# Optimization experiments

Measured on AMD Instinct MI355X. Metric: run time of the kernel, lower is better.

## Reference

```python
import jax, jax.numpy as jnp
import numpy as np


def setup_inputs() -> dict:
    key = jax.random.key(0)
    kq, kk, kv = jax.random.split(key, 3)
    B, S, H, D = 2, 2048, 32, 128
    q = jax.random.normal(kq, (B, S, H, D), dtype=jnp.float32)
    k = jax.random.normal(kk, (B, S, H, D), dtype=jnp.float32)
    v = jax.random.normal(kv, (B, S, H, D), dtype=jnp.float32)
    return {"q": q, "k": k, "v": v}


def _causal_attention(q, k, v):
    # q,k,v: [B, S, H, D] (flash-attn layout). Zigzag ring attention computes
    # exactly standard causal attention; zigzag only balances work across ranks.
    B, S, H, D = q.shape
    scale = 1.0 / jnp.sqrt(jnp.asarray(D, q.dtype))
    scores = jnp.einsum('bqhd,bkhd->bhqk', q, k) * scale  # [B,H,S,S]
    causal = jnp.tril(jnp.ones((S, S), dtype=bool))
    scores = jnp.where(causal, scores, jnp.finfo(scores.dtype).min)
    probs = jax.nn.softmax(scores, axis=-1)
    return jnp.einsum('bhqk,bkhd->bqhd', probs, v)  # [B,S,H,D]


def reference(q, k, v):
    out = _causal_attention(q, k, v)
    return jnp.sum(out)
```

## Files before the change

kernel.cpp:

```cpp
#include <hip/hip_runtime.h>
#include <hip/hip_bf16.h>
#include <stdint.h>

#define B_ 2
#define S_ 2048
#define H_ 32
#define D_ 128
#define R_ (B_*H_*S_)
#define PG 2048
#define CPB 40

typedef __bf16 bf16x8 __attribute__((ext_vector_type(8)));
typedef float  f32x16 __attribute__((ext_vector_type(16)));

#if __has_builtin(__builtin_amdgcn_exp2f)
#define EXP2F(x) __builtin_amdgcn_exp2f(x)
#else
#define EXP2F(x) exp2f(x)
#endif

#define AS1 __attribute__((address_space(1)))
#define AS3 __attribute__((address_space(3)))

__device__ __forceinline__ unsigned short f2bf(float f) {
  unsigned u = __float_as_uint(f);
  u += 0x7FFFu + ((u >> 16) & 1u);
  return (unsigned short)(u >> 16);
}

__global__ __launch_bounds__(256) void prep(
    const float* __restrict__ qf, const float* __restrict__ kf,
    const float* __restrict__ v,
    unsigned short* __restrict__ qc, unsigned short* __restrict__ kc,
    float* __restrict__ vsum, float* __restrict__ nd, float* __restrict__ out0) {
  const int bid = blockIdx.x;
  const int t = threadIdx.x;
  if (bid == 0 && t == 0) out0[0] = 0.f;
  const float sc = 0.0883883476483184f * 1.4426950408889634f;

  #pragma unroll
  for (int g = 0; g < 4; ++g) {
    const size_t i = (size_t)g * (PG * 256) + (size_t)bid * 256 + t;
    const float4 a = *reinterpret_cast<const float4*>(qf + i * 8);
    const float4 b = *reinterpret_cast<const float4*>(qf + i * 8 + 4);
    union { unsigned short u[8]; uint4 v4; } o;
    o.u[0] = f2bf(a.x * sc); o.u[1] = f2bf(a.y * sc);
    o.u[2] = f2bf(a.z * sc); o.u[3] = f2bf(a.w * sc);
    o.u[4] = f2bf(b.x * sc); o.u[5] = f2bf(b.y * sc);
    o.u[6] = f2bf(b.z * sc); o.u[7] = f2bf(b.w * sc);
    *reinterpret_cast<uint4*>(qc + i * 8) = o.v4;
  }
  #pragma unroll
  for (int g = 0; g < 4; ++g) {
    const size_t i = (size_t)g * (PG * 256) + (size_t)bid * 256 + t;
    const float4 a = *reinterpret_cast<const float4*>(kf + i * 8);
    const float4 b = *reinterpret_cast<const float4*>(kf + i * 8 + 4);
    union { unsigned short u[8]; uint4 v4; } o;
    o.u[0] = f2bf(a.x); o.u[1] = f2bf(a.y);
    o.u[2] = f2bf(a.z); o.u[3] = f2bf(a.w);
    o.u[4] = f2bf(b.x); o.u[5] = f2bf(b.y);
    o.u[6] = f2bf(b.z); o.u[7] = f2bf(b.w);
    *reinterpret_cast<uint4*>(kc + i * 8) = o.v4;
  }

  #pragma unroll
  for (int g = 0; g < (B_ * S_) / PG; ++g) {
    const int u = bid + g * PG;
    const int b = u / S_, s = u % S_;
    const int h = t >> 3, i = t & 7;
    const float* p = v + (((size_t)b * S_ + s) * H_ + h) * D_ + i * 16;
    const float4 a0 = *reinterpret_cast<const float4*>(p + 0);
    const float4 a1 = *reinterpret_cast<const float4*>(p + 4);
    const float4 a2 = *reinterpret_cast<const float4*>(p + 8);
    const float4 a3 = *reinterpret_cast<const float4*>(p + 12);
    float sum = (a0.x+a0.y+a0.z+a0.w) + (a1.x+a1.y+a1.z+a1.w)
              + (a2.x+a2.y+a2.z+a2.w) + (a3.x+a3.y+a3.z+a3.w);
    sum += __shfl_xor(sum, 1);
    sum += __shfl_xor(sum, 2);
    sum += __shfl_xor(sum, 4);
    if (i == 0) vsum[((size_t)b * H_ + h) * S_ + s] = sum;
  }

  if (bid < 256) {
    float4* p = reinterpret_cast<float4*>(nd);
    p[(size_t)bid * 256 + t] = float4{0.f, 0.f, 0.f, 0.f};
  }
}

__global__ __launch_bounds__(256, 4) void attn_sum(
    const unsigned short* __restrict__ qc, const unsigned short* __restrict__ kc,
    const float* __restrict__ vsum, float* __restrict__ numb,
    float* __restrict__ denb) {
  __shared__ uint4 kbuf[4][512];
  __shared__ float vsbuf[4][64];

  const int id = blockIdx.x;
  const int y  = id >> 3;
  const int bh = (id & 7) + 8 * (y / CPB);
  const int c  = y % CPB;

  int qt, h, nch;
  if (c < 4)       { qt = c;                 h = 0;            nch = 1; }
  else if (c < 12) { qt = 4 + ((c - 4) >> 1);  h = (c - 4) & 1;  nch = 2; }
  else if (c < 24) { qt = 8 + (c - 12) / 3;    h = (c - 12) % 3; nch = 3; }
  else             { qt = 12 + ((c - 24) >> 2); h = (c - 24) & 3; nch = 4; }
  const int nkt  = 2 * qt + 2;
  const int bas_ = nkt / nch, rem = nkt % nch;
  const int kt0  = h * bas_ + (h < rem ? h : rem);
  const int kt1  = kt0 + bas_ + (h < rem ? 1 : 0);
  const int st0  = 2 * kt0, st1 = 2 * kt1;

  const int t  = threadIdx.x;
  const int w  = t >> 6;
  const int l  = t & 63;
  const int ln = l & 31, l5 = l >> 5;

  const int b0 = bh >> 5, h0 = bh & 31;
  const int qrow0 = qt * 128 + w * 32;
  const unsigned short* kc0 = kc + ((size_t)b0 * S_ * H_ + h0) * D_;
  const float* vsrc0 = vsum + (size_t)bh * S_;

  bf16x8 qfrag[8];
  {
    const unsigned short* qp =
        qc + (((size_t)b0 * S_ + qrow0 + ln) * H_ + h0) * D_ + l5 * 8;
    #pragma unroll
    for (int kb8 = 0; kb8 < 8; ++kb8)
      qfrag[kb8] = *reinterpret_cast<const bf16x8*>(qp + kb8 * 16);
  }

  auto stage = [&](int st, int slot) {
    #pragma unroll
    for (int j = 0; j < 2; ++j) {
      const int idx = (w * 2 + j) * 64 + l;
      const int r   = idx >> 4;
      const int p   = idx & 15;
      const int cc  = p ^ (r & 15);
      const unsigned short* src = kc0 + (size_t)(st * 32 + r) * (H_ * D_) + cc * 8;
      __builtin_amdgcn_global_load_lds(
          (const AS1 void*)src, (AS3 void*)(&kbuf[slot][idx & ~63]), 16, 0, 0);
    }
    __builtin_amdgcn_global_load_lds(
        (const AS1 void*)(vsrc0 + st * 32 + l), (AS3 void*)(&vsbuf[slot][0]), 4, 0, 0);
  };

  float num[16], den[16];
  #pragma unroll
  for (int r = 0; r < 16; ++r) { num[r] = 0.f; den[r] = 0.f; }

  stage(st0, st0 & 3);
  stage(st0 + 1, (st0 + 1) & 3);

  const int xr = ln & 15;
  for (int st = st0; st < st1; ++st) {
    if (st + 1 < st1) asm volatile("s_waitcnt vmcnt(3)" ::: "memory");
    else              asm volatile("s_waitcnt vmcnt(0)" ::: "memory");
    __builtin_amdgcn_s_barrier();
    if (st + 2 < st1) stage(st + 2, (st + 2) & 3);

    const int kbase = st * 32;
    if (kbase <= qrow0 + 31) {
      const int slot = st & 3;
      const uint4* rowb = &kbuf[slot][ln * 16];
      f32x16 sacc = {0.f,0.f,0.f,0.f,0.f,0.f,0.f,0.f,
                     0.f,0.f,0.f,0.f,0.f,0.f,0.f,0.f};
      __builtin_amdgcn_s_setprio(1);
      #pragma unroll
      for (int kb8 = 0; kb8 < 8; ++kb8) {
        const bf16x8 bf = *reinterpret_cast<const bf16x8*>(&rowb[(kb8 * 2 + l5) ^ xr]);
        sacc = __builtin_amdgcn_mfma_f32_32x32x16_bf16(qfrag[kb8], bf, sacc, 0, 0, 0);
      }
      __builtin_amdgcn_s_setprio(0);
      const float vsv = vsbuf[slot][ln];
      if (kbase + 31 <= qrow0) {
        #pragma unroll
        for (int r = 0; r < 16; ++r) {
          const float e = EXP2F(sacc[r]);
          den[r] += e;
          num[r] = fmaf(e, vsv, num[r]);
        }
      } else {
        const int kgc = kbase + ln;
        #pragma unroll
        for (int r = 0; r < 16; ++r) {
          const int qgr = qrow0 + (r & 3) + 8 * (r >> 2) + 4 * l5;
          const float e = (kgc <= qgr) ? EXP2F(sacc[r]) : 0.f;
          den[r] += e;
          num[r] = fmaf(e, vsv, num[r]);
        }
      }
    }
  }

  #pragma unroll
  for (int m = 1; m < 32; m <<= 1) {
    #pragma unroll
    for (int r = 0; r < 16; ++r) {
      num[r] += __shfl_xor(num[r], m);
      den[r] += __shfl_xor(den[r], m);
    }
  }
  if (ln == 0) {
    float* nrow = numb + (size_t)bh * S_;
    float* drow = denb + (size_t)bh * S_;
    #pragma unroll
    for (int r = 0; r < 16; ++r) {
      const int qgr = qrow0 + (r & 3) + 8 * (r >> 2) + 4 * l5;
      atomicAdd(&nrow[qgr], num[r]);
      atomicAdd(&drow[qgr], den[r]);
    }
  }
}

__global__ __launch_bounds__(256) void finalize(
    const float* __restrict__ numb, const float* __restrict__ denb,
    float* __restrict__ out) {
  const int i = blockIdx.x * 256 + threadIdx.x;
  float c = numb[i] / denb[i];
  #pragma unroll
  for (int m = 1; m < 64; m <<= 1) c += __shfl_xor(c, m);
  __shared__ float ps[4];
  if ((threadIdx.x & 63) == 0) ps[threadIdx.x >> 6] = c;
  __syncthreads();
  if (threadIdx.x == 0) atomicAdd(out, ps[0] + ps[1] + ps[2] + ps[3]);
}

extern "C" void kernel_launch(void* const* d_in, const int* in_sizes, int n_in,
                              void* d_out, int out_size, void* d_ws, size_t ws_size,
                              hipStream_t stream) {
  const float* q = (const float*)d_in[0];
  const float* k = (const float*)d_in[1];
  const float* v = (const float*)d_in[2];
  float* out = (float*)d_out;

  unsigned short* qc = (unsigned short*)d_ws;
  unsigned short* kc = qc + (size_t)R_ * D_;
  float* vsum = (float*)(kc + (size_t)R_ * D_);
  float* numb = vsum + R_;
  float* denb = numb + R_;

  hipLaunchKernelGGL(prep, dim3(PG), dim3(256), 0, stream,
                     q, k, v, qc, kc, vsum, numb, out);
  hipLaunchKernelGGL(attn_sum, dim3(64 * CPB), dim3(256), 0, stream,
                     qc, kc, vsum, numb, denb);
  hipLaunchKernelGGL(finalize, dim3(R_ / 256), dim3(256), 0, stream,
                     numb, denb, out);
}
```

Measured before the change: 121.3 us.

## Process two query tiles per block sharing K tiles, transpose MFMA operands

Each block now handles a pair of query tiles (2g and 2g+1) that share every staged K tile. It loads K fragments into registers once and runs the MFMA against both Q fragment sets. The MFMA operands are swapped so each lane owns one query row, which removes the 5-step cross-lane shuffle reduction and most atomics. The work split is rebalanced to 27 chunks per batch-head, and occupancy drops to 3 blocks per SIMD to make room for the extra registers.

```diff
diff --git a/kernel.cpp b/kernel.cpp
--- a/kernel.cpp
+++ b/kernel.cpp
@@ -8,7 +8,7 @@
 #define D_ 128
 #define R_ (B_*H_*S_)
 #define PG 2048
-#define CPB 40
+#define CPB 27
 
 typedef __bf16 bf16x8 __attribute__((ext_vector_type(8)));
 typedef float  f32x16 __attribute__((ext_vector_type(16)));
@@ -87,7 +87,7 @@
   }
 }
 
-__global__ __launch_bounds__(256, 4) void attn_sum(
+__global__ __launch_bounds__(256, 3) void attn_sum(
     const unsigned short* __restrict__ qc, const unsigned short* __restrict__ kc,
     const float* __restrict__ vsum, float* __restrict__ numb,
     float* __restrict__ denb) {
@@ -99,12 +99,16 @@
   const int bh = (id & 7) + 8 * (y / CPB);
   const int c  = y % CPB;
 
-  int qt, h, nch;
-  if (c < 4)       { qt = c;                 h = 0;            nch = 1; }
-  else if (c < 12) { qt = 4 + ((c - 4) >> 1);  h = (c - 4) & 1;  nch = 2; }
-  else if (c < 24) { qt = 8 + (c - 12) / 3;    h = (c - 12) % 3; nch = 3; }
-  else             { qt = 12 + ((c - 24) >> 2); h = (c - 24) & 3; nch = 4; }
-  const int nkt  = 2 * qt + 2;
+  int g, h, nch;
+  if (c < 1)       { g = 0; h = c;      nch = 1; }
+  else if (c < 3)  { g = 1; h = c - 1;  nch = 2; }
+  else if (c < 5)  { g = 2; h = c - 3;  nch = 2; }
+  else if (c < 8)  { g = 3; h = c - 5;  nch = 3; }
+  else if (c < 12) { g = 4; h = c - 8;  nch = 4; }
+  else if (c < 16) { g = 5; h = c - 12; nch = 4; }
+  else if (c < 21) { g = 6; h = c - 16; nch = 5; }
+  else             { g = 7; h = c - 21; nch = 6; }
+  const int nkt  = 4 * g + 4;
   const int bas_ = nkt / nch, rem = nkt % nch;
   const int kt0  = h * bas_ + (h < rem ? h : rem);
   const int kt1  = kt0 + bas_ + (h < rem ? 1 : 0);
@@ -116,17 +120,22 @@
   const int ln = l & 31, l5 = l >> 5;
 
   const int b0 = bh >> 5, h0 = bh & 31;
-  const int qrow0 = qt * 128 + w * 32;
+  const int qminA = (2 * g) * 128 + w * 32;
+  const int qminB = (2 * g + 1) * 128 + w * 32;
   const unsigned short* kc0 = kc + ((size_t)b0 * S_ * H_ + h0) * D_;
   const float* vsrc0 = vsum + (size_t)bh * S_;
 
-  bf16x8 qfrag[8];
+  bf16x8 qfA[8], qfB[8];
   {
-    const unsigned short* qp =
-        qc + (((size_t)b0 * S_ + qrow0 + ln) * H_ + h0) * D_ + l5 * 8;
+    const unsigned short* qpA =
+        qc + (((size_t)b0 * S_ + qminA + ln) * H_ + h0) * D_ + l5 * 8;
+    const unsigned short* qpB =
+        qc + (((size_t)b0 * S_ + qminB + ln) * H_ + h0) * D_ + l5 * 8;
     #pragma unroll
-    for (int kb8 = 0; kb8 < 8; ++kb8)
-      qfrag[kb8] = *reinterpret_cast<const bf16x8*>(qp + kb8 * 16);
+    for (int kb8 = 0; kb8 < 8; ++kb8) {
+      qfA[kb8] = *reinterpret_cast<const bf16x8*>(qpA + kb8 * 16);
+      qfB[kb8] = *reinterpret_cast<const bf16x8*>(qpB + kb8 * 16);
+    }
   }
 
   auto stage = [&](int st, int slot) {
@@ -144,9 +153,7 @@
         (const AS1 void*)(vsrc0 + st * 32 + l), (AS3 void*)(&vsbuf[slot][0]), 4, 0, 0);
   };
 
-  float num[16], den[16];
-  #pragma unroll
-  for (int r = 0; r < 16; ++r) { num[r] = 0.f; den[r] = 0.f; }
+  float npA = 0.f, dpA = 0.f, npB = 0.f, dpB = 0.f;
 
   stage(st0, st0 & 3);
   stage(st0 + 1, (st0 + 1) & 3);
@@ -159,56 +166,84 @@
     if (st + 2 < st1) stage(st + 2, (st + 2) & 3);
 
     const int kbase = st * 32;
-    if (kbase <= qrow0 + 31) {
+    if (kbase <= qminB + 31) {
       const int slot = st & 3;
       const uint4* rowb = &kbuf[slot][ln * 16];
-      f32x16 sacc = {0.f,0.f,0.f,0.f,0.f,0.f,0.f,0.f,
-                     0.f,0.f,0.f,0.f,0.f,0.f,0.f,0.f};
-      __builtin_amdgcn_s_setprio(1);
+      bf16x8 kf[8];
       #pragma unroll
-      for (int kb8 = 0; kb8 < 8; ++kb8) {
-        const bf16x8 bf = *reinterpret_cast<const bf16x8*>(&rowb[(kb8 * 2 + l5) ^ xr]);
-        sacc = __builtin_amdgcn_mfma_f32_32x32x16_bf16(qfrag[kb8], bf, sacc, 0, 0, 0);
+      for (int kb8 = 0; kb8 < 8; ++kb8)
+        kf[kb8] = *reinterpret_cast<const bf16x8*>(&rowb[(kb8 * 2 + l5) ^ xr]);
+      const float4 vs0 = *reinterpret_cast<const float4*>(&vsbuf[slot][ 0 + 4 * l5]);
+      const float4 vs1 = *reinterpret_cast<const float4*>(&vsbuf[slot][ 8 + 4 * l5]);
+      const float4 vs2 = *reinterpret_cast<const float4*>(&vsbuf[slot][16 + 4 * l5]);
+      const float4 vs3 = *reinterpret_cast<const float4*>(&vsbuf[slot][24 + 4 * l5]);
+      const float vsa[16] = {vs0.x,vs0.y,vs0.z,vs0.w, vs1.x,vs1.y,vs1.z,vs1.w,
+                             vs2.x,vs2.y,vs2.z,vs2.w, vs3.x,vs3.y,vs3.z,vs3.w};
+
+      {
+        f32x16 sacc = {0.f,0.f,0.f,0.f,0.f,0.f,0.f,0.f,
+                       0.f,0.f,0.f,0.f,0.f,0.f,0.f,0.f};
+        __builtin_amdgcn_s_setprio(1);
+        #pragma unroll
+        for (int kb8 = 0; kb8 < 8; ++kb8)
+          sacc = __builtin_amdgcn_mfma_f32_32x32x16_bf16(kf[kb8], qfB[kb8], sacc, 0, 0, 0);
+        __builtin_amdgcn_s_setprio(0);
+        if (kbase + 31 <= qminB) {
+          #pragma unroll
+          for (int r = 0; r < 16; ++r) {
+            const float e = EXP2F(sacc[r]);
+            dpB += e;
+            npB = fmaf(e, vsa[r], npB);
+          }
+        } else {
+          const int qg = qminB + ln;
+          #pragma unroll
+          for (int r = 0; r < 16; ++r) {
+            const int kr = kbase + (r & 3) + 8 * (r >> 2) + 4 * l5;
+            const float e = (kr <= qg) ? EXP2F(sacc[r]) : 0.f;
+            dpB += e;
+            npB = fmaf(e, vsa[r], npB);
+          }
+        }
       }
-      __builtin_amdgcn_s_setprio(0);
-      const float vsv = vsbuf[slot][ln];
-      if (kbase + 31 <= qrow0) {
+      if (kbase <= qminA + 31) {
+        f32x16 sacc = {0.f,0.f,0.f,0.f,0.f,0.f,0.f,0.f,
+                       0.f,0.f,0.f,0.f,0.f,0.f,0.f,0.f};
+        __builtin_amdgcn_s_setprio(1);
         #pragma unroll
-        for (int r = 0; r < 16; ++r) {
-          const float e = EXP2F(sacc[r]);
-          den[r] += e;
-          num[r] = fmaf(e, vsv, num[r]);
-        }
-      } else {
-        const int kgc = kbase + ln;
-        #pragma unroll
-        for (int r = 0; r < 16; ++r) {
-          const int qgr = qrow0 + (r & 3) + 8 * (r >> 2) + 4 * l5;
-          const float e = (kgc <= qgr) ? EXP2F(sacc[r]) : 0.f;
-          den[r] += e;
-          num[r] = fmaf(e, vsv, num[r]);
+        for (int kb8 = 0; kb8 < 8; ++kb8)
+          sacc = __builtin_amdgcn_mfma_f32_32x32x16_bf16(kf[kb8], qfA[kb8], sacc, 0, 0, 0);
+        __builtin_amdgcn_s_setprio(0);
+        if (kbase + 31 <= qminA) {
+          #pragma unroll
+          for (int r = 0; r < 16; ++r) {
+            const float e = EXP2F(sacc[r]);
+            dpA += e;
+            npA = fmaf(e, vsa[r], npA);
+          }
+        } else {
+          const int qg = qminA + ln;
+          #pragma unroll
+          for (int r = 0; r < 16; ++r) {
+            const int kr = kbase + (r & 3) + 8 * (r >> 2) + 4 * l5;
+            const float e = (kr <= qg) ? EXP2F(sacc[r]) : 0.f;
+            dpA += e;
+            npA = fmaf(e, vsa[r], npA);
+          }
         }
       }
     }
   }
 
-  #pragma unroll
-  for (int m = 1; m < 32; m <<= 1) {
-    #pragma unroll
-    for (int r = 0; r < 16; ++r) {
-      num[r] += __shfl_xor(num[r], m);
-      den[r] += __shfl_xor(den[r], m);
-    }
-  }
-  if (ln == 0) {
+  npA += __shfl_xor(npA, 32); dpA += __shfl_xor(dpA, 32);
+  npB += __shfl_xor(npB, 32); dpB += __shfl_xor(dpB, 32);
+  if (l5 == 0) {
     float* nrow = numb + (size_t)bh * S_;
     float* drow = denb + (size_t)bh * S_;
-    #pragma unroll
-    for (int r = 0; r < 16; ++r) {
-      const int qgr = qrow0 + (r & 3) + 8 * (r >> 2) + 4 * l5;
-      atomicAdd(&nrow[qgr], num[r]);
-      atomicAdd(&drow[qgr], den[r]);
-    }
+    atomicAdd(&nrow[qminA + ln], npA);
+    atomicAdd(&drow[qminA + ln], dpA);
+    atomicAdd(&nrow[qminB + ln], npB);
+    atomicAdd(&drow[qminB + ln], dpB);
   }
 }
 
```

Measured after the change: 106.9 us. -11.9%, faster.
